# Performance work log

Measured on AMD Instinct MI355X. Metric: run time of the kernel, lower is better.

## Reference

```python
import jax, jax.numpy as jnp
import numpy as np

N = 100000
E = 1600000
IN_DIM = 128
HID = 128
C = 10
N_INJ = 20000
T_HET = 0.5          # self.hetero_level (set by set_adaptation_from_data)
HP_MAX = 1.0         # highpass_scale_max
INJ_LAM = 0.8        # self.inject_lambda


def setup_inputs() -> dict:
    key = jax.random.key(0)
    ks = jax.random.split(key, 16)
    glorot = lambda k, i, o: jax.random.normal(k, (i, o), jnp.float32) * (2.0 / (i + o)) ** 0.5
    return {
        "x": jax.random.normal(ks[0], (N, IN_DIM), jnp.float32),
        "edge_index": jax.random.randint(ks[1], (2, E), 0, N, jnp.int64),
        "inject_indices": jax.random.randint(ks[2], (N_INJ,), 0, N, jnp.int64),
        "initial_preds": jax.random.uniform(ks[3], (N, C), jnp.float32),
        "W1": glorot(ks[4], IN_DIM, HID), "b1": jnp.zeros((HID,), jnp.float32),
        "W2": glorot(ks[5], HID, HID),   "b2": jnp.zeros((HID,), jnp.float32),
        "Wl1": glorot(ks[6], IN_DIM, HID),
        "Wl2": glorot(ks[7], HID, HID),
        "Wm1": glorot(ks[8], HID, HID), "bm1": jnp.zeros((HID,), jnp.float32),
        "Wm2": glorot(ks[9], HID, C),   "bm2": jnp.zeros((C,), jnp.float32),
    }


def _gcn_norm(edge_index):
    # add self loops, symmetric D^{-1/2} (A+I) D^{-1/2} normalization (PyG GCNConv default)
    loops = jnp.arange(N, dtype=edge_index.dtype)
    src = jnp.concatenate([edge_index[0], loops])
    dst = jnp.concatenate([edge_index[1], loops])
    deg = jax.ops.segment_sum(jnp.ones_like(dst, jnp.float32), dst, num_segments=N)
    dinv = jnp.where(deg > 0, jax.lax.rsqrt(jnp.maximum(deg, 1.0)), 0.0)
    norm = dinv[src] * dinv[dst]  # [E+N]
    return src, dst, norm


def _gcn_conv(x, W, b, src, dst, norm):
    h = x @ W                                   # [N, H]
    msg = h[src] * norm[:, None]                # gather + scale, [E+N, H]
    return jax.ops.segment_sum(msg, dst, num_segments=N) + b


def reference(x, edge_index, inject_indices, initial_preds,
              W1, b1, W2, b2, Wl1, Wl2, Wm1, bm1, Wm2, bm2):
    src, dst, norm = _gcn_norm(edge_index)
    mix = T_HET * HP_MAX

    low1 = _gcn_conv(x, W1, b1, src, dst, norm)
    high1 = x @ Wl1 - low1
    h = jax.nn.relu(low1 + mix * high1)        # dropout: eval mode (identity)

    low2 = _gcn_conv(h, W2, b2, src, dst, norm)
    high2 = h @ Wl2 - low2
    h2 = low2 + mix * high2

    logits = jax.nn.relu(h2 @ Wm1 + bm1) @ Wm2 + bm2   # [N, C]
    # indexed injection: logits[idx] = logits[idx] + lam * preds[idx]
    logits = logits.at[inject_indices].set(
        logits[inject_indices] + INJ_LAM * initial_preds[inject_indices])
    return jax.nn.log_softmax(logits, axis=1)
```

## Files before the change

### kernel.cpp

```cpp
#include <hip/hip_runtime.h>
#include <hip/hip_bf16.h>
#include <math.h>

typedef __attribute__((ext_vector_type(8))) short short8;
typedef __attribute__((ext_vector_type(4))) float f32x4;

#define INJ_LAM 0.8f
#define BSH 9
#define BWD 512

__device__ inline float bf2f(unsigned short s){
  union{unsigned u; float f;} v; v.u=((unsigned)s)<<16; return v.f;
}
__device__ inline unsigned short f2bf(float f){
  __hip_bfloat16 h=__float2bfloat16(f);
  return *reinterpret_cast<unsigned short*>(&h);
}
__device__ inline unsigned pack2(float lo, float hi){
  return ((unsigned)f2bf(hi)<<16)|(unsigned)f2bf(lo);
}

__global__ void k_bhist(const int* __restrict__ dst, unsigned* __restrict__ bhist8,
                        const int* __restrict__ inj, unsigned char* __restrict__ flag,
                        int E, int NI){
  __shared__ unsigned lh[256];
  int t=threadIdx.x;
  lh[t]=0u;
  int i=blockIdx.x*256+t;
  if(i<NI) flag[inj[i]]=1;
  __syncthreads();
  int base=blockIdx.x*2048;
  #pragma unroll
  for(int k=0;k<8;k++){
    int e=base+k*256+t;
    if(e<E) atomicAdd(&lh[dst[e]>>BSH],1u);
  }
  __syncthreads();
  if(lh[t]) atomicAdd(&bhist8[t*8],lh[t]);
}

__global__ void k_bscan(const unsigned* __restrict__ bhist8, unsigned* __restrict__ bbase,
                        unsigned* __restrict__ bcur8, int NBK){
  __shared__ unsigned ss[256];
  int t=threadIdx.x;
  unsigned v=(t<NBK)?bhist8[t*8]:0u;
  ss[t]=v; __syncthreads();
  for(int off=1;off<256;off<<=1){
    unsigned u=(t>=off)?ss[t-off]:0u; __syncthreads();
    ss[t]+=u; __syncthreads();
  }
  unsigned excl=ss[t]-v;
  if(t<NBK){ bbase[t]=excl; bcur8[t*8]=excl; }
  if(t==255) bbase[NBK]=ss[255];
}

__global__ void k_bscatter(const int* __restrict__ src, const int* __restrict__ dst,
                           unsigned* __restrict__ bcur8,
                           int* __restrict__ psrc, int* __restrict__ pdst, int E){
  __shared__ unsigned lh[256];
  __shared__ unsigned gb[256];
  int t=threadIdx.x;
  lh[t]=0u; __syncthreads();
  int base=blockIdx.x*2048;
  unsigned lr[8]; int bk[8], sv[8], dv_[8];
  #pragma unroll
  for(int k=0;k<8;k++){
    int e=base+k*256+t;
    if(e<E){
      int d=dst[e]; int b=d>>BSH;
      bk[k]=b; dv_[k]=d; sv[k]=src[e];
      lr[k]=atomicAdd(&lh[b],1u);
    } else bk[k]=-1;
  }
  __syncthreads();
  if(lh[t]) gb[t]=atomicAdd(&bcur8[t*8],lh[t]);
  __syncthreads();
  #pragma unroll
  for(int k=0;k<8;k++){
    if(bk[k]>=0){
      unsigned p=gb[bk[k]]+lr[k];
      psrc[p]=sv[k]; pdst[p]=dv_[k];
    }
  }
}

__launch_bounds__(256)
__global__ void k_bucket(const int* __restrict__ psrc, const int* __restrict__ pdst,
                         const unsigned* __restrict__ bbase, unsigned* __restrict__ rank,
                         unsigned* __restrict__ cnt, unsigned* __restrict__ offs,
                         float* __restrict__ dinv, int* __restrict__ csr, int N){
  __shared__ unsigned lc[BWD];
  __shared__ unsigned lo[BWD];
  __shared__ unsigned ss[256];
  int b=blockIdx.x, t=threadIdx.x;
  unsigned e0=bbase[b], e1=bbase[b+1];
  int lo_node=b<<BSH;
  lc[t]=0u; lc[t+256]=0u; __syncthreads();
  for(unsigned p=e0+t;p<e1;p+=256){
    int dl=pdst[p]-lo_node;
    rank[p]=atomicAdd(&lc[dl],1u);
  }
  __syncthreads();
  unsigned c0=lc[2*t], c1=lc[2*t+1], ps=c0+c1;
  ss[t]=ps; __syncthreads();
  for(int off=1;off<256;off<<=1){
    unsigned u=(t>=off)?ss[t-off]:0u; __syncthreads();
    ss[t]+=u; __syncthreads();
  }
  unsigned excl=ss[t]-ps;
  lo[2*t]=excl; lo[2*t+1]=excl+c0;
  __syncthreads();
  #pragma unroll
  for(int k=0;k<2;k++){
    int nl=t+k*256; int node=lo_node+nl;
    if(node<N){
      unsigned c=lc[nl];
      cnt[node]=c;
      offs[node]=e0+lo[nl];
      dinv[node]=rsqrtf((float)(c+1u));
    }
  }
  for(unsigned p=e0+t;p<e1;p+=256){
    int dl=pdst[p]-lo_node;
    csr[e0+lo[dl]+rank[p]]=psrc[p];
  }
}

__global__ void k_prepw(const float* __restrict__ W1,const float* __restrict__ Wl1,
                        const float* __restrict__ W2,const float* __restrict__ Wl2,
                        const float* __restrict__ Wm1,const float* __restrict__ Wm2,
                        unsigned short* __restrict__ Wt1, unsigned short* __restrict__ Wt2,
                        unsigned short* __restrict__ Wm1t, unsigned short* __restrict__ Wm2tp){
  int i=blockIdx.x*blockDim.x+threadIdx.x;
  if(i<256*128){
    int c=i>>7, k=i&127;
    float v1=(c<128)?W1[k*128+c]:Wl1[k*128+(c-128)];
    float v2=(c<128)?W2[k*128+c]:Wl2[k*128+(c-128)];
    Wt1[i]=f2bf(v1); Wt2[i]=f2bf(v2);
    if(c<128) Wm1t[i]=f2bf(Wm1[k*128+c]);
    if(c<16)  Wm2tp[i]=f2bf((c<10)?Wm2[k*10+c]:0.f);
  }
}

template<bool FP32IN>
__device__ inline void load_afrag(const void* __restrict__ Xv, size_t arow, int l4, short8* a){
  if(FP32IN){
    const float* X=(const float*)Xv + arow*128 + l4*8;
    #pragma unroll
    for(int ks=0;ks<4;ks++){
      float4 f0=*reinterpret_cast<const float4*>(X+ks*32);
      float4 f1=*reinterpret_cast<const float4*>(X+ks*32+4);
      short8 t;
      t[0]=(short)f2bf(f0.x); t[1]=(short)f2bf(f0.y); t[2]=(short)f2bf(f0.z); t[3]=(short)f2bf(f0.w);
      t[4]=(short)f2bf(f1.x); t[5]=(short)f2bf(f1.y); t[6]=(short)f2bf(f1.z); t[7]=(short)f2bf(f1.w);
      a[ks]=t;
    }
  }else{
    const unsigned short* X=(const unsigned short*)Xv + arow*128 + l4*8;
    #pragma unroll
    for(int ks=0;ks<4;ks++)
      a[ks]=*reinterpret_cast<const short8*>(X+ks*32);
  }
}

template<bool FP32IN>
__launch_bounds__(256, 4)
__global__ void k_gemm(const void* __restrict__ Xv, const unsigned short* __restrict__ Wt,
                       const float* __restrict__ dinv,
                       unsigned short* __restrict__ G, unsigned short* __restrict__ XL, int N){
  int wave=threadIdx.x>>6, lane=threadIdx.x&63;
  int l15=lane&15, l4=lane>>4;
  int blk0=blockIdx.x*128;
  if(blk0>=N) return;
  short8 wf[4][4];
  #pragma unroll
  for(int i=0;i<4;i++){
    int col=(wave*4+i)*16+l15;
    #pragma unroll
    for(int ks=0;ks<4;ks++)
      wf[i][ks]=*reinterpret_cast<const short8*>(Wt+(size_t)col*128+ks*32+l4*8);
  }
  int r0=blk0+l15; if(r0>N-1) r0=N-1;
  short8 aC[4], aN[4];
  load_afrag<FP32IN>(Xv,(size_t)r0,l4,aC);
  #pragma unroll 1
  for(int nt=0;nt<8;nt++){
    int node0=blk0+nt*16;
    if(node0>=N) break;
    if(nt<7){
      int rn=node0+16+l15; if(rn>N-1) rn=N-1;
      load_afrag<FP32IN>(Xv,(size_t)rn,l4,aN);
    }
    f32x4 acc[4];
    #pragma unroll
    for(int i=0;i<4;i++) acc[i]=(f32x4){0.f,0.f,0.f,0.f};
    #pragma unroll
    for(int i=0;i<4;i++){
      #pragma unroll
      for(int ks=0;ks<4;ks++)
        acc[i]=__builtin_amdgcn_mfma_f32_16x16x32_bf16(wf[i][ks],aC[ks],acc[i],0,0,0);
    }
    int node=node0+l15;
    if(node<N){
      if(wave<2){
        float dv=dinv[node];
        #pragma unroll
        for(int i=0;i<4;i++){
          f32x4 v=acc[i];
          uint2 p; p.x=pack2(v[0]*dv,v[1]*dv); p.y=pack2(v[2]*dv,v[3]*dv);
          *reinterpret_cast<uint2*>(G+(size_t)node*128+(wave*4+i)*16+l4*4)=p;
        }
      }else{
        #pragma unroll
        for(int i=0;i<4;i++){
          f32x4 v=acc[i];
          uint2 p; p.x=pack2(v[0],v[1]); p.y=pack2(v[2],v[3]);
          *reinterpret_cast<uint2*>(XL+(size_t)node*128+((wave-2)*4+i)*16+l4*4)=p;
        }
      }
    }
    #pragma unroll
    for(int ks=0;ks<4;ks++) aC[ks]=aN[ks];
  }
}

#define ADDROW(acc,v) do{ \
  unsigned _x=(unsigned)(v).x,_y=(unsigned)(v).y,_z=(unsigned)(v).z,_w=(unsigned)(v).w; \
  acc[0]+=bf2f((unsigned short)(_x&0xffffu)); acc[1]+=bf2f((unsigned short)(_x>>16)); \
  acc[2]+=bf2f((unsigned short)(_y&0xffffu)); acc[3]+=bf2f((unsigned short)(_y>>16)); \
  acc[4]+=bf2f((unsigned short)(_z&0xffffu)); acc[5]+=bf2f((unsigned short)(_z>>16)); \
  acc[6]+=bf2f((unsigned short)(_w&0xffffu)); acc[7]+=bf2f((unsigned short)(_w>>16)); }while(0)

template<bool RELU>
__launch_bounds__(256)
__global__ void k_conv(const unsigned short* __restrict__ G, const unsigned short* __restrict__ XL,
                       const float* __restrict__ bias, const float* __restrict__ dinv,
                       const int* __restrict__ csr, const unsigned* __restrict__ offs,
                       const unsigned* __restrict__ cnt,
                       unsigned short* __restrict__ H, int N){
  int node=blockIdx.x*4+(threadIdx.x>>6);
  if(node>=N) return;
  int lane=threadIdx.x&63;
  int g=lane>>4, li=lane&15;
  const int4* Gv=(const int4*)G;
  const int4 Z={0,0,0,0};
  float acc[8];
  #pragma unroll
  for(int i=0;i<8;i++) acc[i]=0.f;
  if(g==0){
    int4 v=Gv[(size_t)node*16+li];
    ADDROW(acc,v);
  }
  unsigned start=offs[node], deg=cnt[node];
  unsigned j=(unsigned)g;
  int4 v0=Z, v1=Z;
  if(j<deg)   v0=Gv[(size_t)csr[start+j]*16+li];
  if(j+4<deg) v1=Gv[(size_t)csr[start+j+4]*16+li];
  j+=8;
  while(j<deg){
    int4 w0=Gv[(size_t)csr[start+j]*16+li];
    int4 w1=(j+4<deg)?Gv[(size_t)csr[start+j+4]*16+li]:Z;
    ADDROW(acc,v0); ADDROW(acc,v1);
    v0=w0; v1=w1; j+=8;
  }
  ADDROW(acc,v0); ADDROW(acc,v1);
  #pragma unroll
  for(int i=0;i<8;i++){
    acc[i]+=__shfl_xor(acc[i],16,64);
    acc[i]+=__shfl_xor(acc[i],32,64);
  }
  if(g==0){
    float dv=dinv[node];
    float4 b0=*reinterpret_cast<const float4*>(bias+li*8);
    float4 b1=*reinterpret_cast<const float4*>(bias+li*8+4);
    int4 xv=((const int4*)XL)[(size_t)node*16+li];
    float xl[8];
    { unsigned _x=(unsigned)xv.x,_y=(unsigned)xv.y,_z=(unsigned)xv.z,_w=(unsigned)xv.w;
      xl[0]=bf2f((unsigned short)(_x&0xffffu)); xl[1]=bf2f((unsigned short)(_x>>16));
      xl[2]=bf2f((unsigned short)(_y&0xffffu)); xl[3]=bf2f((unsigned short)(_y>>16));
      xl[4]=bf2f((unsigned short)(_z&0xffffu)); xl[5]=bf2f((unsigned short)(_z>>16));
      xl[6]=bf2f((unsigned short)(_w&0xffffu)); xl[7]=bf2f((unsigned short)(_w>>16)); }
    float bb[8]={b0.x,b0.y,b0.z,b0.w,b1.x,b1.y,b1.z,b1.w};
    float r[8];
    #pragma unroll
    for(int i=0;i<8;i++){
      r[i]=0.5f*(dv*acc[i]+bb[i])+0.5f*xl[i];
      if(RELU) r[i]=fmaxf(r[i],0.f);
    }
    int4 o;
    o.x=(int)pack2(r[0],r[1]); o.y=(int)pack2(r[2],r[3]);
    o.z=(int)pack2(r[4],r[5]); o.w=(int)pack2(r[6],r[7]);
    ((int4*)H)[(size_t)node*16+li]=o;
  }
}

__launch_bounds__(256)
__global__ void k_mlp(const unsigned short* __restrict__ H2,
                      const unsigned short* __restrict__ Wm1t,
                      const unsigned short* __restrict__ Wm2tp,
                      const float* __restrict__ bm1, const float* __restrict__ bm2,
                      const unsigned char* __restrict__ flag, const float* __restrict__ preds,
                      float* __restrict__ out, int N){
  __shared__ __align__(16) unsigned short zt[4][16][136];
  __shared__ __align__(16) float lt[4][16][16];
  int wave=threadIdx.x>>6, lane=threadIdx.x&63;
  int l15=lane&15, l4=lane>>4;
  int node0=blockIdx.x*64+wave*16;
  int arow=node0+l15; if(arow>N-1) arow=N-1; if(arow<0) arow=0;
  short8 a[4];
  #pragma unroll
  for(int ks=0;ks<4;ks++)
    a[ks]=*reinterpret_cast<const short8*>(H2+(size_t)arow*128+ks*32+l4*8);
  f32x4 acc[8];
  #pragma unroll
  for(int ct=0;ct<8;ct++) acc[ct]=(f32x4){0.f,0.f,0.f,0.f};
  #pragma unroll
  for(int ct=0;ct<8;ct++){
    #pragma unroll
    for(int ks=0;ks<4;ks++){
      short8 bfr=*reinterpret_cast<const short8*>(Wm1t+(size_t)(ct*16+l15)*128+ks*32+l4*8);
      acc[ct]=__builtin_amdgcn_mfma_f32_16x16x32_bf16(bfr,a[ks],acc[ct],0,0,0);
    }
  }
  #pragma unroll
  for(int ct=0;ct<8;ct++){
    float4 bm=*reinterpret_cast<const float4*>(bm1+ct*16+l4*4);
    uint2 p;
    p.x=pack2(fmaxf(acc[ct][0]+bm.x,0.f),fmaxf(acc[ct][1]+bm.y,0.f));
    p.y=pack2(fmaxf(acc[ct][2]+bm.z,0.f),fmaxf(acc[ct][3]+bm.w,0.f));
    *reinterpret_cast<uint2*>(&zt[wave][l15][ct*16+l4*4])=p;
  }
  __syncthreads();
  short8 a2[4];
  #pragma unroll
  for(int ks=0;ks<4;ks++)
    a2[ks]=*reinterpret_cast<const short8*>(&zt[wave][l15][ks*32+l4*8]);
  f32x4 acc2=(f32x4){0.f,0.f,0.f,0.f};
  #pragma unroll
  for(int ks=0;ks<4;ks++){
    short8 bfr=*reinterpret_cast<const short8*>(Wm2tp+(size_t)l15*128+ks*32+l4*8);
    acc2=__builtin_amdgcn_mfma_f32_16x16x32_bf16(bfr,a2[ks],acc2,0,0,0);
  }
  *reinterpret_cast<f32x4*>(&lt[wave][l15][l4*4])=acc2;
  __syncthreads();
  if(lane<16){
    int node=node0+lane;
    if(node<N){
      float v[10];
      #pragma unroll
      for(int c=0;c<10;c++) v[c]=lt[wave][lane][c]+bm2[c];
      if(flag[node]){
        #pragma unroll
        for(int c=0;c<10;c++) v[c]+=INJ_LAM*preds[(size_t)node*10+c];
      }
      float m=v[0];
      #pragma unroll
      for(int c=1;c<10;c++) m=fmaxf(m,v[c]);
      float s=0.f;
      #pragma unroll
      for(int c=0;c<10;c++) s+=expf(v[c]-m);
      float lse=m+logf(s);
      #pragma unroll
      for(int c=0;c<10;c++) out[(size_t)node*10+c]=v[c]-lse;
    }
  }
}

extern "C" void kernel_launch(void* const* d_in, const int* in_sizes, int n_in,
                              void* d_out, int out_size, void* d_ws, size_t ws_size,
                              hipStream_t stream){
  const float* x    =(const float*)d_in[0];
  const int*   ei   =(const int*)  d_in[1];
  const int*   inj  =(const int*)  d_in[2];
  const float* preds=(const float*)d_in[3];
  const float* W1 =(const float*)d_in[4];  const float* b1 =(const float*)d_in[5];
  const float* W2 =(const float*)d_in[6];  const float* b2 =(const float*)d_in[7];
  const float* Wl1=(const float*)d_in[8];  const float* Wl2=(const float*)d_in[9];
  const float* Wm1=(const float*)d_in[10]; const float* bm1=(const float*)d_in[11];
  const float* Wm2=(const float*)d_in[12]; const float* bm2=(const float*)d_in[13];
  float* out=(float*)d_out;

  const int N  = in_sizes[0]/128;
  const int E  = in_sizes[1]/2;
  const int NI = in_sizes[2];
  const int* srcp = ei;
  const int* dstp = ei+E;
  const int NBK = (N+BWD-1)>>BSH;

  char* w=(char*)d_ws;
  auto carve=[&](size_t sz)->char*{ char* p=w; w+=(sz+255)&~(size_t)255; return p; };
  unsigned short* S0 =(unsigned short*)carve((size_t)N*128*2);
  unsigned short* S1 =(unsigned short*)carve((size_t)N*128*2);
  unsigned short* S2 =(unsigned short*)carve((size_t)N*128*2);
  unsigned short* Wt1=(unsigned short*)carve(256*128*2);
  unsigned short* Wt2=(unsigned short*)carve(256*128*2);
  unsigned short* Wm1t=(unsigned short*)carve(128*128*2);
  unsigned short* Wm2tp=(unsigned short*)carve(16*128*2);
  unsigned* cnt   =(unsigned*)carve((size_t)N*4);
  float*    dinv  =(float*)   carve((size_t)N*4);
  unsigned* offs  =(unsigned*)carve((size_t)N*4);
  int*      csr   =(int*)     carve((size_t)E*4);
  unsigned char* flags=(unsigned char*)carve(((size_t)N+3)&~(size_t)3);
  unsigned* bhist8=(unsigned*)carve(256*8*4);
  unsigned* bcur8 =(unsigned*)carve(256*8*4);
  unsigned* bbase =(unsigned*)carve(257*4);
  (void)ws_size; (void)n_in; (void)out_size;

  int* psrc=(int*)S1;
  int* pdst=psrc+E;
  unsigned* rank=(unsigned*)S2;

  const int T=256;
  const int EB=(E+2047)/2048;
  hipMemsetAsync(bhist8, 0, 256*8*4, stream);
  hipMemsetAsync(flags, 0, (size_t)N, stream);
  hipLaunchKernelGGL(k_bhist, dim3(EB), dim3(T), 0, stream, dstp, bhist8, inj, flags, E, NI);
  hipLaunchKernelGGL(k_bscan, dim3(1), dim3(T), 0, stream, bhist8, bbase, bcur8, NBK);
  hipLaunchKernelGGL(k_bscatter, dim3(EB), dim3(T), 0, stream, srcp, dstp, bcur8, psrc, pdst, E);
  hipLaunchKernelGGL(k_bucket, dim3(NBK), dim3(T), 0, stream, psrc, pdst, bbase, rank,
                     cnt, offs, dinv, csr, N);
  hipLaunchKernelGGL(k_prepw, dim3(128), dim3(T), 0, stream, W1,Wl1,W2,Wl2,Wm1,Wm2, Wt1,Wt2,Wm1t,Wm2tp);

  dim3 gemmGrid((N+127)/128);
  hipLaunchKernelGGL(k_gemm<true>,  gemmGrid, dim3(T), 0, stream, (const void*)x,  Wt1, dinv, S1, S2, N);
  hipLaunchKernelGGL(k_conv<true>,  dim3((N+3)/4), dim3(T), 0, stream, S1, S2, b1, dinv, csr, offs, cnt, S0, N);
  hipLaunchKernelGGL(k_gemm<false>, gemmGrid, dim3(T), 0, stream, (const void*)S0, Wt2, dinv, S1, S2, N);
  hipLaunchKernelGGL(k_conv<false>, dim3((N+3)/4), dim3(T), 0, stream, S1, S2, b2, dinv, csr, offs, cnt, S0, N);
  hipLaunchKernelGGL(k_mlp, dim3((N+63)/64), dim3(T), 0, stream, S0, Wm1t, Wm2tp, bm1, bm2, flags, preds, out, N);
}
```

Before: 353.9 us.

## Pack CSR offset/degree, deepen conv gather prefetch, fold mix scale, shuffle-based softmax

Packs each node's CSR offset and degree into one 32-bit word, so the conv kernel reads one array instead of two. The neighbour gather now keeps four rows in flight instead of two, and unpacks bf16 into packed float2 accumulators. The 0.5 mix factor is folded into the bias, the XL output of the GEMM and the dinv scale, which removes multiplies from the conv epilogue. The MLP softmax now runs across lanes with shuffles, replacing the shared-memory round trip and 16-lane serial loop. The packed word limits edge offsets to 21 bits and degree to 11 bits, and the deeper prefetch raises register use.

```diff
diff --git a/kernel.cpp b/kernel.cpp
--- a/kernel.cpp
+++ b/kernel.cpp
@@ -4,6 +4,7 @@
 
 typedef __attribute__((ext_vector_type(8))) short short8;
 typedef __attribute__((ext_vector_type(4))) float f32x4;
+typedef __attribute__((ext_vector_type(2))) float f32x2;
 
 #define INJ_LAM 0.8f
 #define BSH 9
@@ -87,7 +88,7 @@
 __launch_bounds__(256)
 __global__ void k_bucket(const int* __restrict__ psrc, const int* __restrict__ pdst,
                          const unsigned* __restrict__ bbase, unsigned* __restrict__ rank,
-                         unsigned* __restrict__ cnt, unsigned* __restrict__ offs,
+                         unsigned* __restrict__ meta,
                          float* __restrict__ dinv, int* __restrict__ csr, int N){
   __shared__ unsigned lc[BWD];
   __shared__ unsigned lo[BWD];
@@ -115,8 +116,7 @@
     int nl=t+k*256; int node=lo_node+nl;
     if(node<N){
       unsigned c=lc[nl];
-      cnt[node]=c;
-      offs[node]=e0+lo[nl];
+      meta[node]=(e0+lo[nl])|(c<<21);
       dinv[node]=rsqrtf((float)(c+1u));
     }
   }
@@ -129,8 +129,10 @@
 __global__ void k_prepw(const float* __restrict__ W1,const float* __restrict__ Wl1,
                         const float* __restrict__ W2,const float* __restrict__ Wl2,
                         const float* __restrict__ Wm1,const float* __restrict__ Wm2,
+                        const float* __restrict__ b1,const float* __restrict__ b2,
                         unsigned short* __restrict__ Wt1, unsigned short* __restrict__ Wt2,
-                        unsigned short* __restrict__ Wm1t, unsigned short* __restrict__ Wm2tp){
+                        unsigned short* __restrict__ Wm1t, unsigned short* __restrict__ Wm2tp,
+                        float* __restrict__ bh1, float* __restrict__ bh2){
   int i=blockIdx.x*blockDim.x+threadIdx.x;
   if(i<256*128){
     int c=i>>7, k=i&127;
@@ -139,6 +141,7 @@
     Wt1[i]=f2bf(v1); Wt2[i]=f2bf(v2);
     if(c<128) Wm1t[i]=f2bf(Wm1[k*128+c]);
     if(c<16)  Wm2tp[i]=f2bf((c<10)?Wm2[k*10+c]:0.f);
+    if(i<128){ bh1[i]=0.5f*b1[i]; bh2[i]=0.5f*b2[i]; }
   }
 }
 
@@ -214,7 +217,7 @@
         #pragma unroll
         for(int i=0;i<4;i++){
           f32x4 v=acc[i];
-          uint2 p; p.x=pack2(v[0],v[1]); p.y=pack2(v[2],v[3]);
+          uint2 p; p.x=pack2(v[0]*0.5f,v[1]*0.5f); p.y=pack2(v[2]*0.5f,v[3]*0.5f);
           *reinterpret_cast<uint2*>(XL+(size_t)node*128+((wave-2)*4+i)*16+l4*4)=p;
         }
       }
@@ -224,19 +227,19 @@
   }
 }
 
-#define ADDROW(acc,v) do{ \
-  unsigned _x=(unsigned)(v).x,_y=(unsigned)(v).y,_z=(unsigned)(v).z,_w=(unsigned)(v).w; \
-  acc[0]+=bf2f((unsigned short)(_x&0xffffu)); acc[1]+=bf2f((unsigned short)(_x>>16)); \
-  acc[2]+=bf2f((unsigned short)(_y&0xffffu)); acc[3]+=bf2f((unsigned short)(_y>>16)); \
-  acc[4]+=bf2f((unsigned short)(_z&0xffffu)); acc[5]+=bf2f((unsigned short)(_z>>16)); \
-  acc[6]+=bf2f((unsigned short)(_w&0xffffu)); acc[7]+=bf2f((unsigned short)(_w>>16)); }while(0)
+#define ADDQ(v) do{ \
+  unsigned ux=(unsigned)(v).x, uy=(unsigned)(v).y, uz=(unsigned)(v).z, uw=(unsigned)(v).w; \
+  accv[0]+=(f32x2){__uint_as_float(ux<<16),__uint_as_float(ux&0xffff0000u)}; \
+  accv[1]+=(f32x2){__uint_as_float(uy<<16),__uint_as_float(uy&0xffff0000u)}; \
+  accv[2]+=(f32x2){__uint_as_float(uz<<16),__uint_as_float(uz&0xffff0000u)}; \
+  accv[3]+=(f32x2){__uint_as_float(uw<<16),__uint_as_float(uw&0xffff0000u)}; \
+}while(0)
 
 template<bool RELU>
 __launch_bounds__(256)
 __global__ void k_conv(const unsigned short* __restrict__ G, const unsigned short* __restrict__ XL,
-                       const float* __restrict__ bias, const float* __restrict__ dinv,
-                       const int* __restrict__ csr, const unsigned* __restrict__ offs,
-                       const unsigned* __restrict__ cnt,
+                       const float* __restrict__ bh, const float* __restrict__ dinv,
+                       const int* __restrict__ csr, const unsigned* __restrict__ meta,
                        unsigned short* __restrict__ H, int N){
   int node=blockIdx.x*4+(threadIdx.x>>6);
   if(node>=N) return;
@@ -244,35 +247,44 @@
   int g=lane>>4, li=lane&15;
   const int4* Gv=(const int4*)G;
   const int4 Z={0,0,0,0};
-  float acc[8];
-  #pragma unroll
-  for(int i=0;i<8;i++) acc[i]=0.f;
+  f32x2 accv[4];
+  #pragma unroll
+  for(int i=0;i<4;i++) accv[i]=(f32x2){0.f,0.f};
   if(g==0){
     int4 v=Gv[(size_t)node*16+li];
-    ADDROW(acc,v);
-  }
-  unsigned start=offs[node], deg=cnt[node];
+    ADDQ(v);
+  }
+  unsigned mt=meta[node];
+  unsigned start=mt&0x1FFFFFu, deg=mt>>21;
   unsigned j=(unsigned)g;
-  int4 v0=Z, v1=Z;
-  if(j<deg)   v0=Gv[(size_t)csr[start+j]*16+li];
-  if(j+4<deg) v1=Gv[(size_t)csr[start+j+4]*16+li];
-  j+=8;
+  int4 v0=Z,v1=Z,v2=Z,v3=Z;
+  if(j<deg)    v0=Gv[(size_t)csr[start+j]*16+li];
+  if(j+4<deg)  v1=Gv[(size_t)csr[start+j+4]*16+li];
+  if(j+8<deg)  v2=Gv[(size_t)csr[start+j+8]*16+li];
+  if(j+12<deg) v3=Gv[(size_t)csr[start+j+12]*16+li];
+  j+=16;
   while(j<deg){
-    int4 w0=Gv[(size_t)csr[start+j]*16+li];
-    int4 w1=(j+4<deg)?Gv[(size_t)csr[start+j+4]*16+li]:Z;
-    ADDROW(acc,v0); ADDROW(acc,v1);
-    v0=w0; v1=w1; j+=8;
-  }
-  ADDROW(acc,v0); ADDROW(acc,v1);
+    int4 n0=Z,n1=Z,n2=Z,n3=Z;
+    n0=Gv[(size_t)csr[start+j]*16+li];
+    if(j+4<deg)  n1=Gv[(size_t)csr[start+j+4]*16+li];
+    if(j+8<deg)  n2=Gv[(size_t)csr[start+j+8]*16+li];
+    if(j+12<deg) n3=Gv[(size_t)csr[start+j+12]*16+li];
+    ADDQ(v0); ADDQ(v1); ADDQ(v2); ADDQ(v3);
+    v0=n0; v1=n1; v2=n2; v3=n3; j+=16;
+  }
+  ADDQ(v0); ADDQ(v1); ADDQ(v2); ADDQ(v3);
+  float acc[8];
+  #pragma unroll
+  for(int i=0;i<4;i++){ acc[2*i]=accv[i][0]; acc[2*i+1]=accv[i][1]; }
   #pragma unroll
   for(int i=0;i<8;i++){
     acc[i]+=__shfl_xor(acc[i],16,64);
     acc[i]+=__shfl_xor(acc[i],32,64);
   }
   if(g==0){
-    float dv=dinv[node];
-    float4 b0=*reinterpret_cast<const float4*>(bias+li*8);
-    float4 b1=*reinterpret_cast<const float4*>(bias+li*8+4);
+    float dv2=0.5f*dinv[node];
+    float4 b0=*reinterpret_cast<const float4*>(bh+li*8);
+    float4 b1=*reinterpret_cast<const float4*>(bh+li*8+4);
     int4 xv=((const int4*)XL)[(size_t)node*16+li];
     float xl[8];
     { unsigned _x=(unsigned)xv.x,_y=(unsigned)xv.y,_z=(unsigned)xv.z,_w=(unsigned)xv.w;
@@ -284,7 +296,7 @@
     float r[8];
     #pragma unroll
     for(int i=0;i<8;i++){
-      r[i]=0.5f*(dv*acc[i]+bb[i])+0.5f*xl[i];
+      r[i]=dv2*acc[i]+bb[i]+xl[i];
       if(RELU) r[i]=fmaxf(r[i],0.f);
     }
     int4 o;
@@ -302,7 +314,6 @@
                       const unsigned char* __restrict__ flag, const float* __restrict__ preds,
                       float* __restrict__ out, int N){
   __shared__ __align__(16) unsigned short zt[4][16][136];
-  __shared__ __align__(16) float lt[4][16][16];
   int wave=threadIdx.x>>6, lane=threadIdx.x&63;
   int l15=lane&15, l4=lane>>4;
   int node0=blockIdx.x*64+wave*16;
@@ -341,27 +352,37 @@
     short8 bfr=*reinterpret_cast<const short8*>(Wm2tp+(size_t)l15*128+ks*32+l4*8);
     acc2=__builtin_amdgcn_mfma_f32_16x16x32_bf16(bfr,a2[ks],acc2,0,0,0);
   }
-  *reinterpret_cast<f32x4*>(&lt[wave][l15][l4*4])=acc2;
-  __syncthreads();
-  if(lane<16){
-    int node=node0+lane;
-    if(node<N){
-      float v[10];
-      #pragma unroll
-      for(int c=0;c<10;c++) v[c]=lt[wave][lane][c]+bm2[c];
-      if(flag[node]){
-        #pragma unroll
-        for(int c=0;c<10;c++) v[c]+=INJ_LAM*preds[(size_t)node*10+c];
-      }
-      float m=v[0];
-      #pragma unroll
-      for(int c=1;c<10;c++) m=fmaxf(m,v[c]);
-      float s=0.f;
-      #pragma unroll
-      for(int c=0;c<10;c++) s+=expf(v[c]-m);
-      float lse=m+logf(s);
-      #pragma unroll
-      for(int c=0;c<10;c++) out[(size_t)node*10+c]=v[c]-lse;
+  int node=node0+l15;
+  bool have=node<N;
+  int c0=l4*4;
+  float v[4];
+  #pragma unroll
+  for(int k=0;k<4;k++){
+    int c=c0+k;
+    v[k]=(c<10)?(acc2[k]+bm2[c]):-3.0e38f;
+  }
+  if(have && c0<10 && flag[node]){
+    #pragma unroll
+    for(int k=0;k<4;k++){
+      int c=c0+k;
+      if(c<10) v[k]+=INJ_LAM*preds[(size_t)node*10+c];
+    }
+  }
+  float m=fmaxf(fmaxf(v[0],v[1]),fmaxf(v[2],v[3]));
+  m=fmaxf(m,__shfl_xor(m,16,64));
+  m=fmaxf(m,__shfl_xor(m,32,64));
+  float s=0.f;
+  #pragma unroll
+  for(int k=0;k<4;k++){ int c=c0+k; if(c<10) s+=expf(v[k]-m); }
+  s+=__shfl_xor(s,16,64);
+  s+=__shfl_xor(s,32,64);
+  float lse=m+logf(s);
+  if(have && c0<10){
+    float2 o01; o01.x=v[0]-lse; o01.y=v[1]-lse;
+    *reinterpret_cast<float2*>(out+(size_t)node*10+c0)=o01;
+    if(c0+2<10){
+      float2 o23; o23.x=v[2]-lse; o23.y=v[3]-lse;
+      *reinterpret_cast<float2*>(out+(size_t)node*10+c0+2)=o23;
     }
   }
 }
@@ -396,14 +417,15 @@
   unsigned short* Wt2=(unsigned short*)carve(256*128*2);
   unsigned short* Wm1t=(unsigned short*)carve(128*128*2);
   unsigned short* Wm2tp=(unsigned short*)carve(16*128*2);
-  unsigned* cnt   =(unsigned*)carve((size_t)N*4);
   float*    dinv  =(float*)   carve((size_t)N*4);
-  unsigned* offs  =(unsigned*)carve((size_t)N*4);
+  unsigned* meta  =(unsigned*)carve((size_t)N*4);
   int*      csr   =(int*)     carve((size_t)E*4);
   unsigned char* flags=(unsigned char*)carve(((size_t)N+3)&~(size_t)3);
   unsigned* bhist8=(unsigned*)carve(256*8*4);
   unsigned* bcur8 =(unsigned*)carve(256*8*4);
   unsigned* bbase =(unsigned*)carve(257*4);
+  float* bh1=(float*)carve(128*4);
+  float* bh2=(float*)carve(128*4);
   (void)ws_size; (void)n_in; (void)out_size;
 
   int* psrc=(int*)S1;
@@ -418,13 +440,14 @@
   hipLaunchKernelGGL(k_bscan, dim3(1), dim3(T), 0, stream, bhist8, bbase, bcur8, NBK);
   hipLaunchKernelGGL(k_bscatter, dim3(EB), dim3(T), 0, stream, srcp, dstp, bcur8, psrc, pdst, E);
   hipLaunchKernelGGL(k_bucket, dim3(NBK), dim3(T), 0, stream, psrc, pdst, bbase, rank,
-                     cnt, offs, dinv, csr, N);
-  hipLaunchKernelGGL(k_prepw, dim3(128), dim3(T), 0, stream, W1,Wl1,W2,Wl2,Wm1,Wm2, Wt1,Wt2,Wm1t,Wm2tp);
+                     meta, dinv, csr, N);
+  hipLaunchKernelGGL(k_prepw, dim3(128), dim3(T), 0, stream, W1,Wl1,W2,Wl2,Wm1,Wm2,b1,b2,
+                     Wt1,Wt2,Wm1t,Wm2tp,bh1,bh2);
 
   dim3 gemmGrid((N+127)/128);
   hipLaunchKernelGGL(k_gemm<true>,  gemmGrid, dim3(T), 0, stream, (const void*)x,  Wt1, dinv, S1, S2, N);
-  hipLaunchKernelGGL(k_conv<true>,  dim3((N+3)/4), dim3(T), 0, stream, S1, S2, b1, dinv, csr, offs, cnt, S0, N);
+  hipLaunchKernelGGL(k_conv<true>,  dim3((N+3)/4), dim3(T), 0, stream, S1, S2, bh1, dinv, csr, meta, S0, N);
   hipLaunchKernelGGL(k_gemm<false>, gemmGrid, dim3(T), 0, stream, (const void*)S0, Wt2, dinv, S1, S2, N);
-  hipLaunchKernelGGL(k_conv<false>, dim3((N+3)/4), dim3(T), 0, stream, S1, S2, b2, dinv, csr, offs, cnt, S0, N);
+  hipLaunchKernelGGL(k_conv<false>, dim3((N+3)/4), dim3(T), 0, stream, S1, S2, bh2, dinv, csr, meta, S0, N);
   hipLaunchKernelGGL(k_mlp, dim3((N+63)/64), dim3(T), 0, stream, S0, Wm1t, Wm2tp, bm1, bm2, flags, preds, out, N);
 }
```

New measurement: 346.7 us. 1.02x faster.
